# Performance work log

Measured on AMD Instinct MI355X. Metric: run time of the kernel, lower is better.

Reference implementation:

```python
import jax, jax.numpy as jnp
import numpy as np

PARA_CH = 256
FEATURE_CH = 256
PI = 3.14159  # matches the literal in the torch source


def _linear_params(key, fan_in, fan_out):
    kw, kb = jax.random.split(key)
    bound = 1.0 / np.sqrt(fan_in)
    W = jax.random.uniform(kw, (fan_in, fan_out), minval=-bound, maxval=bound, dtype=jnp.float32)
    b = jax.random.uniform(kb, (fan_out,), minval=-bound, maxval=bound, dtype=jnp.float32)
    return W, b


def setup_inputs() -> dict:
    key = jax.random.key(0)
    ks = jax.random.split(key, 6)
    feature_map = jax.random.normal(ks[0], (4, FEATURE_CH, 128, 128), dtype=jnp.float32)
    para_code = jax.random.normal(ks[1], (4, PARA_CH), dtype=jnp.float32)
    W1, b1 = _linear_params(ks[2], PARA_CH, PARA_CH)
    Ws, bs = _linear_params(ks[3], PARA_CH, FEATURE_CH)
    Wr, br = _linear_params(ks[4], PARA_CH, FEATURE_CH)
    Wt, bt = _linear_params(ks[5], PARA_CH, 2 * FEATURE_CH)
    return {"feature_map": feature_map, "para_code": para_code,
            "W1": W1, "b1": b1, "Ws": Ws, "bs": bs,
            "Wr": Wr, "br": br, "Wt": Wt, "bt": bt}


def _coord_1d(n):
    # align_corners=True-style normalized coordinates, as in make_coordinate_grid_3d
    return 2.0 * (jnp.arange(n, dtype=jnp.float32) / (n - 1)) - 1.0


def _trilinear_sample_zeros(vol, gx, gy, gz):
    """F.grid_sample 5D equivalent: mode='bilinear' (trilinear), padding_mode='zeros',
    align_corners=False. vol: [B,D,H,W] (channel dim of size 1 squeezed out);
    gx,gy,gz: [B,Do,Ho,Wo] normalized coords. Returns [B,Do,Ho,Wo]."""
    B, D, H, W = vol.shape
    ix = ((gx + 1.0) * W - 1.0) * 0.5
    iy = ((gy + 1.0) * H - 1.0) * 0.5
    iz = ((gz + 1.0) * D - 1.0) * 0.5
    x0f, y0f, z0f = jnp.floor(ix), jnp.floor(iy), jnp.floor(iz)
    wx, wy, wz = ix - x0f, iy - y0f, iz - z0f
    x0 = x0f.astype(jnp.int32); x1 = x0 + 1
    y0 = y0f.astype(jnp.int32); y1 = y0 + 1
    z0 = z0f.astype(jnp.int32); z1 = z0 + 1
    vflat = vol.reshape(B, -1)

    def gather(zi, yi, xi):
        valid = (zi >= 0) & (zi < D) & (yi >= 0) & (yi < H) & (xi >= 0) & (xi < W)
        zc = jnp.clip(zi, 0, D - 1)
        yc = jnp.clip(yi, 0, H - 1)
        xc = jnp.clip(xi, 0, W - 1)
        flat = (zc * H + yc) * W + xc  # [B,Do,Ho,Wo]
        v = jnp.take_along_axis(vflat, flat.reshape(B, -1), axis=1).reshape(flat.shape)
        return jnp.where(valid, v, 0.0)

    out = (gather(z0, y0, x0) * (1 - wz) * (1 - wy) * (1 - wx)
           + gather(z0, y0, x1) * (1 - wz) * (1 - wy) * wx
           + gather(z0, y1, x0) * (1 - wz) * wy * (1 - wx)
           + gather(z0, y1, x1) * (1 - wz) * wy * wx
           + gather(z1, y0, x0) * wz * (1 - wy) * (1 - wx)
           + gather(z1, y0, x1) * wz * (1 - wy) * wx
           + gather(z1, y1, x0) * wz * wy * (1 - wx)
           + gather(z1, y1, x1) * wz * wy * wx)
    return out


def reference(feature_map, para_code, W1, b1, Ws, bs, Wr, br, Wt, bt):
    B, C, H, W = feature_map.shape  # C == feature_ch == depth of 3D grid
    p = jax.nn.relu(para_code @ W1 + b1)                      # [B, para_ch]
    scale = jax.nn.sigmoid(p @ Ws + bs) * 2.0                 # [B, C]
    angle = jnp.tanh(p @ Wr + br) * PI                        # [B, C]
    translation = jnp.tanh(p @ Wt + bt).reshape(B, C, 2)      # [B, C, 2]
    ca, sa = jnp.cos(angle), jnp.sin(angle)
    # rotation matrix [[cos, -sin], [sin, cos]] per (batch, channel)
    rot = jnp.stack([jnp.stack([ca, -sa], -1), jnp.stack([sa, ca], -1)], -2)  # [B,C,2,2]

    x = _coord_1d(W)  # [W]
    y = _coord_1d(H)  # [H]
    z = _coord_1d(C)  # [C] (depth == channel dim)
    grid_xy = jnp.stack(jnp.broadcast_arrays(x[None, None, :], y[None, :, None]), -1)  # [1,H,W,2] -> broadcast to [C,H,W,2]
    grid_xy = jnp.broadcast_to(grid_xy, (C, H, W, 2))

    # per-pixel affine transform: rot @ [x,y] * scale + trans
    trans_grid = jnp.einsum('bcij,chwj->bchwi', rot, grid_xy)
    trans_grid = trans_grid * scale[:, :, None, None, None] + translation[:, :, None, None, :]
    gx = trans_grid[..., 0]
    gy = trans_grid[..., 1]
    gz = jnp.broadcast_to(z[None, :, None, None], (B, C, H, W))

    return _trilinear_sample_zeros(feature_map, gx, gy, gz)  # [B,C,H,W]
```

## Files before the change

### kernel.cpp

```cpp
#include <hip/hip_runtime.h>
#include <math.h>

#define BATCH 4
#define CH    256
#define HH    128
#define WW    128
#define PC    256
#define PI_F  3.14159f
#define PLANE (HH * WW)

#define PSTRIDE 134
#define PROWS   131
#define BUFSZ   (PROWS * PSTRIDE)
#define NBORDER 1170

__device__ __forceinline__ void barrier_lds() {
    asm volatile("s_waitcnt lgkmcnt(0)\n\ts_barrier" ::: "memory");
}

struct Stage { float4 a[4]; float4 b[4]; };

__device__ __forceinline__ Stage stage_load(const float* __restrict__ pl0,
                                            const float* __restrict__ pl1, int t) {
    Stage s;
#pragma unroll
    for (int j = 0; j < 4; ++j) {
        const int f = 4 * (t + 1024 * j);
        s.a[j] = *(const float4*)(pl0 + f);
        s.b[j] = *(const float4*)(pl1 + f);
    }
    return s;
}

__device__ __forceinline__ void stage_store_pad(float* __restrict__ buf, const Stage& s,
                                                float wz0, float wz1, int t) {
#pragma unroll
    for (int j = 0; j < 4; ++j) {
        const int f = 4 * (t + 1024 * j);
        const int y = f >> 7, x = f & (WW - 1);
        float* p = &buf[(y + 1) * PSTRIDE + (x + 1)];
        p[0] = fmaf(wz0, s.a[j].x, wz1 * s.b[j].x);
        p[1] = fmaf(wz0, s.a[j].y, wz1 * s.b[j].y);
        p[2] = fmaf(wz0, s.a[j].z, wz1 * s.b[j].z);
        p[3] = fmaf(wz0, s.a[j].w, wz1 * s.b[j].w);
    }
}

__global__ __launch_bounds__(1024)
void adaat_params_kernel(const float* __restrict__ pc,
                         const float* __restrict__ W1, const float* __restrict__ b1,
                         const float* __restrict__ Ws, const float* __restrict__ bs,
                         const float* __restrict__ Wr, const float* __restrict__ br,
                         const float* __restrict__ Wt, const float* __restrict__ bt,
                         float4* __restrict__ par) {
    __shared__ float red[1024];
    __shared__ float p_sh[PC];
    __shared__ float hd[4][PC];

    const int t = threadIdx.x;
    const int b = blockIdx.x;

    {
        const int jj = t & 255, kk = t >> 8;
        const float* pcb = pc + b * PC + kk * 64;
        const float* w   = W1 + (kk * 64) * PC + jj;
        float acc = 0.0f;
#pragma unroll 8
        for (int i = 0; i < 64; ++i)
            acc = fmaf(pcb[i], w[i * PC], acc);
        red[t] = acc;
    }
    __syncthreads();
    if (t < 256)
        p_sh[t] = fmaxf(red[t] + red[256 + t] + red[512 + t] + red[768 + t] + b1[t], 0.0f);
    __syncthreads();

    {
        const int c = t & 255, h = t >> 8;
        const float* wp; int stride;
        if      (h == 0) { wp = Ws + c;                stride = PC;     }
        else if (h == 1) { wp = Wr + c;                stride = PC;     }
        else             { wp = Wt + 2 * c + (h == 3); stride = 2 * PC; }
        float dot = 0.0f;
#pragma unroll 8
        for (int k = 0; k < PC; ++k)
            dot = fmaf(p_sh[k], wp[(size_t)k * stride], dot);
        hd[h][c] = dot;
    }
    __syncthreads();

    if (t < 256) {
        const int c = t;
        const float s2  = 2.0f / (1.0f + expf(-(hd[0][c] + bs[c])));
        const float ang = tanhf(hd[1][c] + br[c]) * PI_F;
        float sa, ca;
        sincosf(ang, &sa, &ca);
        const float A  = s2 * ca, B = s2 * sa;
        const float Tx = tanhf(hd[2][c] + bt[2 * c]);
        const float Ty = tanhf(hd[3][c] + bt[2 * c + 1]);
        par[b * 256 + c] = make_float4(A * (128.0f / 127.0f),
                                       B * (128.0f / 127.0f),
                                       64.0f * (Tx - A + B) + 64.5f,
                                       64.0f * (Ty - A - B) + 64.5f);
    }
}

__global__ __launch_bounds__(1024, 8)
void adaat_fused_kernel(const float* __restrict__ fm,
                        const float4* __restrict__ par,
                        float* __restrict__ out) {
    __shared__ float lds[BUFSZ];

    const int t = threadIdx.x;

    const int bid = blockIdx.x;
    const int lc  = ((bid & 7) << 7) | (bid >> 3);
    const int b   = lc >> 8;
    const int c   = lc & (CH - 1);

    const float* base = fm + (size_t)b * (CH * PLANE);
    const float  iz = (256.0f / 255.0f) * (float)c - 0.5f;
    const float  zf = floorf(iz);
    const float  fz = iz - zf;
    const int    z0 = (int)zf;
    const float  w0 = (z0 >= 0)     ? (1.0f - fz) : 0.0f;
    const float  w1 = (z0 + 1 < CH) ? fz          : 0.0f;
    const float* pl0 = base + (size_t)max(z0, 0)          * PLANE;
    const float* pl1 = base + (size_t)min(z0 + 1, CH - 1) * PLANE;

    Stage s = stage_load(pl0, pl1, t);

    const float4 P = par[lc];

#pragma unroll
    for (int i = t; i < NBORDER; i += 1024) {
        int row, col;
        if (i < 402) {
            row = i / 134;
            if (row == 1) row = 129; else if (row == 2) row = 130;
            col = i % 134;
        } else {
            const int j = i - 402;
            row = 1 + j / 6;
            const int cs = j % 6;
            col = (cs == 0) ? 0 : 128 + cs;
        }
        lds[row * PSTRIDE + col] = 0.0f;
    }

    stage_store_pad(lds, s, w0, w1, t);

    barrier_lds();

    {
        const int    wv = t >> 6, l = t & 63;
        const float  cA = P.x, cB = P.y;
        float* outp = out + (size_t)lc * PLANE;
        const float xf0 = (float)l;
        float rowf = (float)(wv * 8);
#pragma unroll 2
        for (int r = 0; r < 8; ++r) {
            const float bx = fmaf(-cB, rowf, P.z);
            const float by = fmaf( cA, rowf, P.w);
            float* orow = outp + (wv * 8 + r) * WW;
#pragma unroll
            for (int h = 0; h < 2; ++h) {
                const float xf  = xf0 + 64.0f * h;
                const float ix  = fmaf(cA, xf, bx);
                const float iy  = fmaf(cB, xf, by);
                const float xc  = fminf(fmaxf(ix, 0.0f), 129.99f);
                const float yc  = fminf(fmaxf(iy, 0.0f), 129.99f);
                const float x0f = floorf(xc), y0f = floorf(yc);
                const float fx  = xc - x0f,   fy  = yc - y0f;
                const int   a   = (int)y0f * PSTRIDE + (int)x0f;
                const float v00 = lds[a],           v01 = lds[a + 1];
                const float v10 = lds[a + PSTRIDE], v11 = lds[a + PSTRIDE + 1];
                const float h0  = fmaf(fx, v01 - v00, v00);
                const float h1  = fmaf(fx, v11 - v10, v10);
                orow[h * 64 + l] = fmaf(fy, h1 - h0, h0);
            }
            rowf += 1.0f;
        }
    }
}

extern "C" void kernel_launch(void* const* d_in, const int* in_sizes, int n_in,
                              void* d_out, int out_size, void* d_ws, size_t ws_size,
                              hipStream_t stream) {
    const float* feature_map = (const float*)d_in[0];
    const float* para_code   = (const float*)d_in[1];
    const float* W1 = (const float*)d_in[2];
    const float* b1 = (const float*)d_in[3];
    const float* Ws = (const float*)d_in[4];
    const float* bs = (const float*)d_in[5];
    const float* Wr = (const float*)d_in[6];
    const float* br = (const float*)d_in[7];
    const float* Wt = (const float*)d_in[8];
    const float* bt = (const float*)d_in[9];

    float4* par = (float4*)d_ws;

    adaat_params_kernel<<<BATCH, 1024, 0, stream>>>(
        para_code, W1, b1, Ws, bs, Wr, br, Wt, bt, par);

    adaat_fused_kernel<<<BATCH * CH, 1024, 0, stream>>>(
        feature_map, par, (float*)d_out);
}
```

Baseline: 161.9 us.

## Split parameter MLP into two kernels and move activations into fused kernel

The single 4-block parameter kernel is split in two. The first kernel computes the hidden layer. The second runs 16 blocks, each covering one head and batch, with a K-split reduction, so the serial 256-long dot products become parallel 64-long partial sums. The sigmoid/tanh/sincos epilogue now runs in thread 0 of each fused block and is shared through LDS. This adds a kernel launch and per-block transcendental work, but removes the long serial latency of the tiny parameter kernel.

```diff
diff --git a/kernel.cpp b/kernel.cpp
--- a/kernel.cpp
+++ b/kernel.cpp
@@ -13,6 +13,11 @@
 #define PROWS   131
 #define BUFSZ   (PROWS * PSTRIDE)
 #define NBORDER 1170
+
+#define WS_P    0
+#define WS_S    1024
+#define WS_R    2048
+#define WS_T    3072
 
 __device__ __forceinline__ void barrier_lds() {
     asm volatile("s_waitcnt lgkmcnt(0)\n\ts_barrier" ::: "memory");
@@ -47,19 +52,12 @@
 }
 
 __global__ __launch_bounds__(1024)
-void adaat_params_kernel(const float* __restrict__ pc,
-                         const float* __restrict__ W1, const float* __restrict__ b1,
-                         const float* __restrict__ Ws, const float* __restrict__ bs,
-                         const float* __restrict__ Wr, const float* __restrict__ br,
-                         const float* __restrict__ Wt, const float* __restrict__ bt,
-                         float4* __restrict__ par) {
+void adaat_p1_kernel(const float* __restrict__ pc,
+                     const float* __restrict__ W1, const float* __restrict__ b1,
+                     float* __restrict__ ws) {
     __shared__ float red[1024];
-    __shared__ float p_sh[PC];
-    __shared__ float hd[4][PC];
-
     const int t = threadIdx.x;
     const int b = blockIdx.x;
-
     {
         const int jj = t & 255, kk = t >> 8;
         const float* pcb = pc + b * PC + kk * 64;
@@ -72,44 +70,52 @@
     }
     __syncthreads();
     if (t < 256)
-        p_sh[t] = fmaxf(red[t] + red[256 + t] + red[512 + t] + red[768 + t] + b1[t], 0.0f);
+        ws[WS_P + b * 256 + t] =
+            fmaxf(red[t] + red[256 + t] + red[512 + t] + red[768 + t] + b1[t], 0.0f);
+}
+
+__global__ __launch_bounds__(1024)
+void adaat_p2_kernel(const float* __restrict__ Ws,
+                     const float* __restrict__ Wr,
+                     const float* __restrict__ Wt,
+                     float* __restrict__ ws) {
+    __shared__ float red[1024];
+    __shared__ float p_sh[PC];
+    const int t = threadIdx.x;
+    const int b = blockIdx.x >> 2;
+    const int g = blockIdx.x & 3;
+
+    if (t < 256) p_sh[t] = ws[WS_P + b * 256 + t];
     __syncthreads();
 
-    {
-        const int c = t & 255, h = t >> 8;
-        const float* wp; int stride;
-        if      (h == 0) { wp = Ws + c;                stride = PC;     }
-        else if (h == 1) { wp = Wr + c;                stride = PC;     }
-        else             { wp = Wt + 2 * c + (h == 3); stride = 2 * PC; }
-        float dot = 0.0f;
+    const int o = t & 255, kk = t >> 8;
+    const float* wp; int stride; int dst;
+    if      (g == 0) { wp = Ws + o;       stride = PC;     dst = WS_S + b * 256 + o;       }
+    else if (g == 1) { wp = Wr + o;       stride = PC;     dst = WS_R + b * 256 + o;       }
+    else if (g == 2) { wp = Wt + o;       stride = 2 * PC; dst = WS_T + b * 512 + o;       }
+    else             { wp = Wt + 256 + o; stride = 2 * PC; dst = WS_T + b * 512 + 256 + o; }
+
+    float acc = 0.0f;
+    const float* pk = p_sh + kk * 64;
+    const float* wk = wp + (size_t)(kk * 64) * stride;
 #pragma unroll 8
-        for (int k = 0; k < PC; ++k)
-            dot = fmaf(p_sh[k], wp[(size_t)k * stride], dot);
-        hd[h][c] = dot;
-    }
+    for (int i = 0; i < 64; ++i)
+        acc = fmaf(pk[i], wk[(size_t)i * stride], acc);
+    red[t] = acc;
     __syncthreads();
-
-    if (t < 256) {
-        const int c = t;
-        const float s2  = 2.0f / (1.0f + expf(-(hd[0][c] + bs[c])));
-        const float ang = tanhf(hd[1][c] + br[c]) * PI_F;
-        float sa, ca;
-        sincosf(ang, &sa, &ca);
-        const float A  = s2 * ca, B = s2 * sa;
-        const float Tx = tanhf(hd[2][c] + bt[2 * c]);
-        const float Ty = tanhf(hd[3][c] + bt[2 * c + 1]);
-        par[b * 256 + c] = make_float4(A * (128.0f / 127.0f),
-                                       B * (128.0f / 127.0f),
-                                       64.0f * (Tx - A + B) + 64.5f,
-                                       64.0f * (Ty - A - B) + 64.5f);
-    }
+    if (t < 256)
+        ws[dst] = red[t] + red[256 + t] + red[512 + t] + red[768 + t];
 }
 
 __global__ __launch_bounds__(1024, 8)
 void adaat_fused_kernel(const float* __restrict__ fm,
-                        const float4* __restrict__ par,
+                        const float* __restrict__ ws,
+                        const float* __restrict__ bs,
+                        const float* __restrict__ br,
+                        const float* __restrict__ bt,
                         float* __restrict__ out) {
-    __shared__ float lds[BUFSZ];
+    __shared__ float  lds[BUFSZ];
+    __shared__ float4 sh_par;
 
     const int t = threadIdx.x;
 
@@ -130,7 +136,23 @@
 
     Stage s = stage_load(pl0, pl1, t);
 
-    const float4 P = par[lc];
+    if (t == 0) {
+        const float ds  = ws[WS_S + lc];
+        const float dr  = ws[WS_R + lc];
+        const float dt0 = ws[WS_T + b * 512 + 2 * c];
+        const float dt1 = ws[WS_T + b * 512 + 2 * c + 1];
+        const float s2  = 2.0f / (1.0f + expf(-(ds + bs[c])));
+        const float ang = tanhf(dr + br[c]) * PI_F;
+        float sa, ca;
+        sincosf(ang, &sa, &ca);
+        const float A  = s2 * ca, B = s2 * sa;
+        const float Tx = tanhf(dt0 + bt[2 * c]);
+        const float Ty = tanhf(dt1 + bt[2 * c + 1]);
+        sh_par = make_float4(A * (128.0f / 127.0f),
+                             B * (128.0f / 127.0f),
+                             64.0f * (Tx - A + B) + 64.5f,
+                             64.0f * (Ty - A - B) + 64.5f);
+    }
 
 #pragma unroll
     for (int i = t; i < NBORDER; i += 1024) {
@@ -154,6 +176,7 @@
 
     {
         const int    wv = t >> 6, l = t & 63;
+        const float4 P  = sh_par;
         const float  cA = P.x, cB = P.y;
         float* outp = out + (size_t)lc * PLANE;
         const float xf0 = (float)l;
@@ -198,11 +221,10 @@
     const float* Wt = (const float*)d_in[8];
     const float* bt = (const float*)d_in[9];
 
-    float4* par = (float4*)d_ws;
-
-    adaat_params_kernel<<<BATCH, 1024, 0, stream>>>(
-        para_code, W1, b1, Ws, bs, Wr, br, Wt, bt, par);
-
+    float* ws = (float*)d_ws;
+
+    adaat_p1_kernel<<<BATCH, 1024, 0, stream>>>(para_code, W1, b1, ws);
+    adaat_p2_kernel<<<4 * BATCH, 1024, 0, stream>>>(Ws, Wr, Wt, ws);
     adaat_fused_kernel<<<BATCH * CH, 1024, 0, stream>>>(
-        feature_map, par, (float*)d_out);
-}
+        feature_map, ws, bs, br, bt, (float*)d_out);
+}
```

Result: faster. 143.7 us (-11.2%).
